# Performance work log

Hardware: AMD Instinct MI355X
Metric: run time of the kernel (lower is better)

## Reference

```python
import jax, jax.numpy as jnp
import numpy as np

DIM = 512
NUM_HEADS = 16
WIN = (7, 7)
SIZE = WIN[0] * WIN[1]  # 49
B = 2048   # total windows
NW = 4     # windows per image (mask groups)


def _relative_position_index():
    coords_h = np.arange(WIN[0])
    coords_w = np.arange(WIN[1])
    coords = np.stack(np.meshgrid(coords_h, coords_w, indexing='ij'))  # [2,Wh,Ww]
    flat = coords.reshape(2, -1)                                       # [2,S]
    rel = flat[:, :, None] - flat[:, None, :]                          # [2,S,S]
    rel = rel.transpose(1, 2, 0)                                       # [S,S,2]
    rel[:, :, 0] += WIN[0] - 1
    rel[:, :, 1] += WIN[1] - 1
    rel[:, :, 0] *= 2 * WIN[1] - 1
    return rel.sum(-1).astype(np.int32)                                # [S,S]


def setup_inputs() -> dict:
    key = jax.random.key(0)
    ks = jax.random.split(key, 8)
    num_bias = (2 * WIN[0] - 1) * (2 * WIN[1] - 1)  # 169
    sd = 1.0 / np.sqrt(DIM)
    return {
        'x': jax.random.normal(ks[0], (B, SIZE, DIM), dtype=jnp.float32),
        'mask': jax.random.normal(ks[1], (NW, SIZE, SIZE), dtype=jnp.float32),
        'w_qkv': jax.random.normal(ks[2], (DIM, 3 * DIM), dtype=jnp.float32) * sd,
        'b_qkv': jnp.zeros((3 * DIM,), dtype=jnp.float32),
        'w_proj': jax.random.normal(ks[3], (DIM, DIM), dtype=jnp.float32) * sd,
        'b_proj': jnp.zeros((DIM,), dtype=jnp.float32),
        'bias_table': jax.random.normal(ks[4], (num_bias, NUM_HEADS), dtype=jnp.float32) * 0.02,
        'rel_idx': jnp.asarray(_relative_position_index()),
    }


def reference(x, mask, w_qkv, b_qkv, w_proj, b_proj, bias_table, rel_idx):
    b, s, c = x.shape
    h = NUM_HEADS
    hd = c // h
    scale = hd ** (-0.5)
    # qkv projection -> [3, B, H, S, hd]
    qkv = (x @ w_qkv + b_qkv).reshape(b, s, 3, h, hd).transpose(2, 0, 3, 1, 4)
    q, k, v = qkv[0] * scale, qkv[1], qkv[2]
    attn = jnp.einsum('bhqd,bhkd->bhqk', q, k)                 # [B,H,S,S]
    # gathered relative position bias -> [H,S,S]
    bias = bias_table[rel_idx.reshape(-1)].reshape(s, s, h).transpose(2, 0, 1)
    attn = attn + bias[None]
    nw = mask.shape[0]
    attn = attn.reshape(b // nw, nw, h, s, s) + mask[None, :, None]
    attn = jax.nn.softmax(attn.reshape(b, h, s, s), axis=-1)
    out = jnp.einsum('bhqk,bhkd->bhqd', attn, v)               # [B,H,S,hd]
    out = out.transpose(0, 2, 1, 3).reshape(b, s, c)
    return out @ w_proj + b_proj
```

## Files before the change

### kernel.cpp

```cpp
#include <hip/hip_runtime.h>
#include <hip/hip_bf16.h>
#include <stdint.h>

typedef float  floatx4 __attribute__((ext_vector_type(4)));
typedef short  short8  __attribute__((ext_vector_type(8)));
typedef unsigned short u16;

#define DIM 512
#define NH 16
#define HD 32
#define WS 49
#define NBW 2048
#define NWIN 4
#define M_TOTAL (NBW*WS)
#define N_QKV (3*DIM)

__device__ __forceinline__ u16 f2bf(float f) {
    uint32_t u = __float_as_uint(f);
    u += 0x7FFFu + ((u >> 16) & 1u);
    return (u16)(u >> 16);
}

__device__ __forceinline__ void load_lds16(const u16* g, u16* l) {
    __builtin_amdgcn_global_load_lds(
        (const __attribute__((address_space(1))) unsigned int*)g,
        (__attribute__((address_space(3))) unsigned int*)l, 16, 0, 0);
}

__global__ void cast_x_kernel(const float* __restrict__ in, u16* __restrict__ out, int n4) {
    int i = blockIdx.x * blockDim.x + threadIdx.x;
    if (i >= n4) return;
    const float4 v = ((const float4*)in)[i];
    ushort4 o;
    o.x = f2bf(v.x); o.y = f2bf(v.y); o.z = f2bf(v.z); o.w = f2bf(v.w);
    ((ushort4*)out)[i] = o;
}

__global__ void transpose_cast_kernel(const float* __restrict__ in, u16* __restrict__ out,
                                      int N, int total) {
    int idx = blockIdx.x * blockDim.x + threadIdx.x;
    if (idx >= total) return;
    int k = idx & (DIM - 1);
    int n = idx >> 9;
    out[idx] = f2bf(in[k * N + n]);
}

__global__ void build_comb_kernel(const float* __restrict__ bias_table, const int* __restrict__ rel_idx,
                                  const float* __restrict__ mask, float* __restrict__ comb) {
    int idx = blockIdx.x * blockDim.x + threadIdx.x;
    if (idx >= NWIN * NH * 64 * 64) return;
    int j = idx & 63, i = (idx >> 6) & 63, h = (idx >> 12) & 15, g = idx >> 16;
    float v = -1e30f;
    if (i < WS && j < WS)
        v = bias_table[rel_idx[i * WS + j] * NH + h] + mask[(g * WS + i) * WS + j];
    comb[idx] = v;
}

template<bool OUT_BF16>
__global__ __launch_bounds__(256, 2) void gemm_bt_kernel(
    const u16* __restrict__ A, const u16* __restrict__ Bt,
    const float* __restrict__ bias, void* __restrict__ out, int N, int K)
{
    __shared__ __align__(16) u16 sA[128 * 32];
    __shared__ __align__(16) u16 sB[128 * 32];
    const int tid  = threadIdx.x;
    const int lane = tid & 63;
    const int wave = tid >> 6;
    const long m0 = (long)blockIdx.y * 128;
    const long n0 = (long)blockIdx.x * 128;
    const int rr = lane & 15;
    const int qk = (lane >> 4) * 8;
    const int wm = (wave >> 1) * 64;
    const int wn = (wave & 1) * 64;

    floatx4 acc[4][4];
    const floatx4 z4 = {0.f, 0.f, 0.f, 0.f};
#pragma unroll
    for (int mi = 0; mi < 4; ++mi)
#pragma unroll
        for (int ni = 0; ni < 4; ++ni) acc[mi][ni] = z4;

    const int row0 = tid >> 2;
    const int kc0  = (tid & 3) * 8;
    const u16* gA0 = A  + (m0 + row0) * K + kc0;
    const u16* gA1 = A  + (m0 + row0 + 64) * K + kc0;
    const u16* gB0 = Bt + (n0 + row0) * K + kc0;
    const u16* gB1 = Bt + (n0 + row0 + 64) * K + kc0;
    u16* lA0 = sA + tid * 8;
    u16* lA1 = sA + (tid + 256) * 8;
    u16* lB0 = sB + tid * 8;
    u16* lB1 = sB + (tid + 256) * 8;

    for (int k0 = 0; k0 < K; k0 += 32) {
        load_lds16(gA0 + k0, lA0);
        load_lds16(gA1 + k0, lA1);
        load_lds16(gB0 + k0, lB0);
        load_lds16(gB1 + k0, lB1);
        __syncthreads();
        short8 af[4], bfr[4];
#pragma unroll
        for (int mi = 0; mi < 4; ++mi)
            af[mi] = *(const short8*)(sA + (wm + mi * 16 + rr) * 32 + qk);
#pragma unroll
        for (int ni = 0; ni < 4; ++ni)
            bfr[ni] = *(const short8*)(sB + (wn + ni * 16 + rr) * 32 + qk);
#pragma unroll
        for (int mi = 0; mi < 4; ++mi)
#pragma unroll
            for (int ni = 0; ni < 4; ++ni)
                acc[mi][ni] = __builtin_amdgcn_mfma_f32_16x16x32_bf16(af[mi], bfr[ni], acc[mi][ni], 0, 0, 0);
        __syncthreads();
    }

#pragma unroll
    for (int mi = 0; mi < 4; ++mi) {
#pragma unroll
        for (int r = 0; r < 4; ++r) {
            const long m = m0 + wm + mi * 16 + (lane >> 4) * 4 + r;
#pragma unroll
            for (int ni = 0; ni < 4; ++ni) {
                const long n = n0 + wn + ni * 16 + rr;
                float v = acc[mi][ni][r] + bias[n];
                if (OUT_BF16) ((u16*)out)[m * N + n] = f2bf(v);
                else          ((float*)out)[m * N + n] = v;
            }
        }
    }
}

__global__ __launch_bounds__(64, 4) void attn_kernel(
    const u16* __restrict__ qkv, const float* __restrict__ comb,
    u16* __restrict__ attn_out)
{
    const int bh = blockIdx.x;
    const int b = bh >> 4, h = bh & 15;
    const int l = threadIdx.x;
    const int rr = l & 15;
    const int q4 = l >> 4;
    const int qk = q4 * 8;

    __shared__ __align__(16) u16 p_s[64 * 64];

    const u16* qg = qkv + (long)b * WS * N_QKV + h * HD;
    const u16* kg = qg + DIM;
    const u16* vg = qg + 2 * DIM;

    short8 af[4], bfr[4];
    const short8 z8 = {0, 0, 0, 0, 0, 0, 0, 0};
#pragma unroll
    for (int mi = 0; mi < 4; ++mi) {
        const int row = mi * 16 + rr;
        af[mi] = (row < WS) ? *(const short8*)(qg + (long)row * N_QKV + qk) : z8;
    }
#pragma unroll
    for (int ni = 0; ni < 4; ++ni) {
        const int row = ni * 16 + rr;
        bfr[ni] = (row < WS) ? *(const short8*)(kg + (long)row * N_QKV + qk) : z8;
    }

    floatx4 sc[4][4];
    const floatx4 z4 = {0.f, 0.f, 0.f, 0.f};
#pragma unroll
    for (int mi = 0; mi < 4; ++mi)
#pragma unroll
        for (int ni = 0; ni < 4; ++ni)
            sc[mi][ni] = __builtin_amdgcn_mfma_f32_16x16x32_bf16(af[mi], bfr[ni], z4, 0, 0, 0);

    short8 vf[2][2];
#pragma unroll
    for (int kk = 0; kk < 2; ++kk)
#pragma unroll
        for (int ni = 0; ni < 2; ++ni) {
            short8 t = z8;
            const int d = ni * 16 + rr;
#pragma unroll
            for (int j = 0; j < 8; ++j) {
                const int s = kk * 32 + qk + j;
                if (s < WS) t[j] = (short)vg[(long)s * N_QKV + d];
            }
            vf[kk][ni] = t;
        }

    const float* cb = comb + (long)((b & (NWIN - 1)) * NH + h) * 4096;
    const float scale = 0.17677669529663689f;
    float inv_s[4][4];
#pragma unroll
    for (int mi = 0; mi < 4; ++mi) {
#pragma unroll
        for (int r = 0; r < 4; ++r) {
            const int i = mi * 16 + q4 * 4 + r;
            float s0 = sc[mi][0][r] * scale + cb[i * 64 +  0 + rr];
            float s1 = sc[mi][1][r] * scale + cb[i * 64 + 16 + rr];
            float s2 = sc[mi][2][r] * scale + cb[i * 64 + 32 + rr];
            float s3 = sc[mi][3][r] * scale + cb[i * 64 + 48 + rr];
            float mx = fmaxf(fmaxf(s0, s1), fmaxf(s2, s3));
#pragma unroll
            for (int off = 1; off < 16; off <<= 1) mx = fmaxf(mx, __shfl_xor(mx, off, 64));
            float e0 = __expf(s0 - mx), e1 = __expf(s1 - mx);
            float e2 = __expf(s2 - mx), e3 = __expf(s3 - mx);
            float sm = e0 + e1 + e2 + e3;
#pragma unroll
            for (int off = 1; off < 16; off <<= 1) sm += __shfl_xor(sm, off, 64);
            inv_s[mi][r] = 1.0f / sm;
#pragma unroll
            for (int c = 0; c < 4; ++c) {
                const int col = c * 16 + rr;
                const int blk = (col >> 3) ^ (i & 7);
                const float ev = (c == 0) ? e0 : (c == 1) ? e1 : (c == 2) ? e2 : e3;
                p_s[i * 64 + blk * 8 + (col & 7)] = f2bf(ev);
            }
        }
    }
    __syncthreads();

    floatx4 oacc[4][2];
#pragma unroll
    for (int mi = 0; mi < 4; ++mi) { oacc[mi][0] = z4; oacc[mi][1] = z4; }
#pragma unroll
    for (int kk = 0; kk < 2; ++kk) {
        short8 pf[4];
#pragma unroll
        for (int mi = 0; mi < 4; ++mi) {
            const int i2 = mi * 16 + rr;
            pf[mi] = *(const short8*)(p_s + i2 * 64 + (((4 * kk + q4) ^ (i2 & 7)) * 8));
        }
#pragma unroll
        for (int mi = 0; mi < 4; ++mi)
#pragma unroll
            for (int ni = 0; ni < 2; ++ni)
                oacc[mi][ni] = __builtin_amdgcn_mfma_f32_16x16x32_bf16(pf[mi], vf[kk][ni], oacc[mi][ni], 0, 0, 0);
    }

#pragma unroll
    for (int mi = 0; mi < 4; ++mi) {
#pragma unroll
        for (int r = 0; r < 4; ++r) {
            const int i = mi * 16 + q4 * 4 + r;
            if (i < WS) {
                const float inv = inv_s[mi][r];
                u16* op = attn_out + ((long)(b * WS + i)) * DIM + h * HD;
                op[rr]      = f2bf(oacc[mi][0][r] * inv);
                op[16 + rr] = f2bf(oacc[mi][1][r] * inv);
            }
        }
    }
}

extern "C" void kernel_launch(void* const* d_in, const int* in_sizes, int n_in,
                              void* d_out, int out_size, void* d_ws, size_t ws_size,
                              hipStream_t stream)
{
    const float* x          = (const float*)d_in[0];
    const float* mask       = (const float*)d_in[1];
    const float* w_qkv      = (const float*)d_in[2];
    const float* b_qkv      = (const float*)d_in[3];
    const float* w_proj     = (const float*)d_in[4];
    const float* b_proj     = (const float*)d_in[5];
    const float* bias_table = (const float*)d_in[6];
    const int*   rel_idx    = (const int*)d_in[7];
    float* out = (float*)d_out;

    char* ws = (char*)d_ws;
    u16* x_bf   = (u16*)ws;  ws += (size_t)M_TOTAL * DIM * 2;
    u16* wqkvT  = (u16*)ws;  ws += (size_t)N_QKV * DIM * 2;
    u16* wprojT = (u16*)ws;  ws += (size_t)DIM * DIM * 2;
    float* comb = (float*)ws; ws += (size_t)NWIN * NH * 64 * 64 * 4;
    u16* qkv    = (u16*)ws;  ws += (size_t)M_TOTAL * N_QKV * 2;
    u16* attn_o = x_bf;

    const int n4 = M_TOTAL * DIM / 4;
    cast_x_kernel<<<(n4 + 255) / 256, 256, 0, stream>>>(x, x_bf, n4);
    transpose_cast_kernel<<<(N_QKV * DIM + 255) / 256, 256, 0, stream>>>(w_qkv, wqkvT, N_QKV, N_QKV * DIM);
    transpose_cast_kernel<<<(DIM * DIM + 255) / 256, 256, 0, stream>>>(w_proj, wprojT, DIM, DIM * DIM);
    build_comb_kernel<<<(NWIN * NH * 64 * 64 + 255) / 256, 256, 0, stream>>>(bias_table, rel_idx, mask, comb);

    gemm_bt_kernel<true><<<dim3(N_QKV / 128, M_TOTAL / 128), 256, 0, stream>>>(
        x_bf, wqkvT, b_qkv, qkv, N_QKV, DIM);

    attn_kernel<<<NBW * NH, 64, 0, stream>>>(qkv, comb, attn_o);

    gemm_bt_kernel<false><<<dim3(DIM / 128, M_TOTAL / 128), 256, 0, stream>>>(
        attn_o, wprojT, b_proj, out, DIM, DIM);
}
```

Before: 905.7 us.

## Split attention per half-window per wave, drop max-subtraction, compute row sums via MFMA

The attention kernel now gives each wave half the query rows of one (window, head) pair and packs four waves per block. This halves per-wave register and LDS use and replaces the block barrier with an LDS wait. Softmax no longer subtracts the row max, and the row sum comes from an extra MFMA against a ones vector instead of shuffle reductions. The comb table is reordered so each lane reads a float4, and the output stores are packed into 32-bit words. Skipping max-subtraction risks exp overflow with larger logits, and K and V fragments are now loaded twice per window.

After: 856.5 us. 1.06x faster.

```diff
diff --git a/kernel.cpp b/kernel.cpp
--- a/kernel.cpp
+++ b/kernel.cpp
@@ -49,7 +49,8 @@
                                   const float* __restrict__ mask, float* __restrict__ comb) {
     int idx = blockIdx.x * blockDim.x + threadIdx.x;
     if (idx >= NWIN * NH * 64 * 64) return;
-    int j = idx & 63, i = (idx >> 6) & 63, h = (idx >> 12) & 15, g = idx >> 16;
+    int c = idx & 3, jj = (idx >> 2) & 15, i = (idx >> 6) & 63, h = (idx >> 12) & 15, g = idx >> 16;
+    int j = c * 16 + jj;
     float v = -1e30f;
     if (i < WS && j < WS)
         v = bias_table[rel_idx[i * WS + j] * NH + h] + mask[(g * WS + i) * WS + j];
@@ -128,28 +129,35 @@
     }
 }
 
-__global__ __launch_bounds__(64, 4) void attn_kernel(
+__global__ __launch_bounds__(256, 4) void attn_kernel(
     const u16* __restrict__ qkv, const float* __restrict__ comb,
     u16* __restrict__ attn_out)
 {
-    const int bh = blockIdx.x;
-    const int b = bh >> 4, h = bh & 15;
-    const int l = threadIdx.x;
+    const int w   = threadIdx.x >> 6;
+    const int l   = threadIdx.x & 63;
+    const int job = blockIdx.x * 4 + w;
+    const int b    = job >> 5;
+    const int h    = (job >> 1) & 15;
+    const int half = job & 1;
+    const int row0 = half * 32;
     const int rr = l & 15;
     const int q4 = l >> 4;
     const int qk = q4 * 8;
 
-    __shared__ __align__(16) u16 p_s[64 * 64];
+    __shared__ __align__(16) u16 p_s[4][32 * 64];
+    u16* ps = p_s[w];
 
     const u16* qg = qkv + (long)b * WS * N_QKV + h * HD;
     const u16* kg = qg + DIM;
     const u16* vg = qg + 2 * DIM;
 
-    short8 af[4], bfr[4];
     const short8 z8 = {0, 0, 0, 0, 0, 0, 0, 0};
-#pragma unroll
-    for (int mi = 0; mi < 4; ++mi) {
-        const int row = mi * 16 + rr;
+    const floatx4 z4 = {0.f, 0.f, 0.f, 0.f};
+
+    short8 af[2], bfr[4];
+#pragma unroll
+    for (int mi = 0; mi < 2; ++mi) {
+        const int row = row0 + mi * 16 + rr;
         af[mi] = (row < WS) ? *(const short8*)(qg + (long)row * N_QKV + qk) : z8;
     }
 #pragma unroll
@@ -158,21 +166,13 @@
         bfr[ni] = (row < WS) ? *(const short8*)(kg + (long)row * N_QKV + qk) : z8;
     }
 
-    floatx4 sc[4][4];
-    const floatx4 z4 = {0.f, 0.f, 0.f, 0.f};
-#pragma unroll
-    for (int mi = 0; mi < 4; ++mi)
-#pragma unroll
-        for (int ni = 0; ni < 4; ++ni)
-            sc[mi][ni] = __builtin_amdgcn_mfma_f32_16x16x32_bf16(af[mi], bfr[ni], z4, 0, 0, 0);
-
     short8 vf[2][2];
 #pragma unroll
     for (int kk = 0; kk < 2; ++kk)
 #pragma unroll
         for (int ni = 0; ni < 2; ++ni) {
             short8 t = z8;
-            const int d = ni * 16 + rr;
+            const int d = 2 * rr + ni;
 #pragma unroll
             for (int j = 0; j < 8; ++j) {
                 const int s = kk * 32 + qk + j;
@@ -180,67 +180,70 @@
             }
             vf[kk][ni] = t;
         }
-
-    const float* cb = comb + (long)((b & (NWIN - 1)) * NH + h) * 4096;
+    short8 vones;
+#pragma unroll
+    for (int j = 0; j < 8; ++j) vones[j] = (short)0x3F80;
+
+    floatx4 sc[2][4];
+#pragma unroll
+    for (int mi = 0; mi < 2; ++mi)
+#pragma unroll
+        for (int ni = 0; ni < 4; ++ni)
+            sc[mi][ni] = __builtin_amdgcn_mfma_f32_16x16x32_bf16(af[mi], bfr[ni], z4, 0, 0, 0);
+
+    const float4* cb4 = (const float4*)comb + ((long)((b & (NWIN - 1)) * NH + h)) * 1024;
     const float scale = 0.17677669529663689f;
-    float inv_s[4][4];
-#pragma unroll
-    for (int mi = 0; mi < 4; ++mi) {
+#pragma unroll
+    for (int mi = 0; mi < 2; ++mi) {
 #pragma unroll
         for (int r = 0; r < 4; ++r) {
-            const int i = mi * 16 + q4 * 4 + r;
-            float s0 = sc[mi][0][r] * scale + cb[i * 64 +  0 + rr];
-            float s1 = sc[mi][1][r] * scale + cb[i * 64 + 16 + rr];
-            float s2 = sc[mi][2][r] * scale + cb[i * 64 + 32 + rr];
-            float s3 = sc[mi][3][r] * scale + cb[i * 64 + 48 + rr];
-            float mx = fmaxf(fmaxf(s0, s1), fmaxf(s2, s3));
-#pragma unroll
-            for (int off = 1; off < 16; off <<= 1) mx = fmaxf(mx, __shfl_xor(mx, off, 64));
-            float e0 = __expf(s0 - mx), e1 = __expf(s1 - mx);
-            float e2 = __expf(s2 - mx), e3 = __expf(s3 - mx);
-            float sm = e0 + e1 + e2 + e3;
-#pragma unroll
-            for (int off = 1; off < 16; off <<= 1) sm += __shfl_xor(sm, off, 64);
-            inv_s[mi][r] = 1.0f / sm;
+            const int il = mi * 16 + q4 * 4 + r;
+            const float4 cb = cb4[(row0 + il) * 16 + rr];
+            float e0 = __expf(sc[mi][0][r] * scale + cb.x);
+            float e1 = __expf(sc[mi][1][r] * scale + cb.y);
+            float e2 = __expf(sc[mi][2][r] * scale + cb.z);
+            float e3 = __expf(sc[mi][3][r] * scale + cb.w);
 #pragma unroll
             for (int c = 0; c < 4; ++c) {
                 const int col = c * 16 + rr;
-                const int blk = (col >> 3) ^ (i & 7);
+                const int blk = (col >> 3) ^ (il & 7);
                 const float ev = (c == 0) ? e0 : (c == 1) ? e1 : (c == 2) ? e2 : e3;
-                p_s[i * 64 + blk * 8 + (col & 7)] = f2bf(ev);
-            }
-        }
-    }
-    __syncthreads();
-
-    floatx4 oacc[4][2];
-#pragma unroll
-    for (int mi = 0; mi < 4; ++mi) { oacc[mi][0] = z4; oacc[mi][1] = z4; }
+                ps[il * 64 + blk * 8 + (col & 7)] = f2bf(ev);
+            }
+        }
+    }
+    asm volatile("s_waitcnt lgkmcnt(0)" ::: "memory");
+
+    floatx4 oacc[2][3];
+#pragma unroll
+    for (int mi = 0; mi < 2; ++mi) { oacc[mi][0] = z4; oacc[mi][1] = z4; oacc[mi][2] = z4; }
 #pragma unroll
     for (int kk = 0; kk < 2; ++kk) {
-        short8 pf[4];
-#pragma unroll
-        for (int mi = 0; mi < 4; ++mi) {
+        short8 pf[2];
+#pragma unroll
+        for (int mi = 0; mi < 2; ++mi) {
             const int i2 = mi * 16 + rr;
-            pf[mi] = *(const short8*)(p_s + i2 * 64 + (((4 * kk + q4) ^ (i2 & 7)) * 8));
-        }
-#pragma unroll
-        for (int mi = 0; mi < 4; ++mi)
-#pragma unroll
-            for (int ni = 0; ni < 2; ++ni)
-                oacc[mi][ni] = __builtin_amdgcn_mfma_f32_16x16x32_bf16(pf[mi], vf[kk][ni], oacc[mi][ni], 0, 0, 0);
-    }
-
-#pragma unroll
-    for (int mi = 0; mi < 4; ++mi) {
+            pf[mi] = *(const short8*)(ps + i2 * 64 + (((4 * kk + q4) ^ (i2 & 7)) * 8));
+        }
+#pragma unroll
+        for (int mi = 0; mi < 2; ++mi) {
+            oacc[mi][0] = __builtin_amdgcn_mfma_f32_16x16x32_bf16(pf[mi], vf[kk][0], oacc[mi][0], 0, 0, 0);
+            oacc[mi][1] = __builtin_amdgcn_mfma_f32_16x16x32_bf16(pf[mi], vf[kk][1], oacc[mi][1], 0, 0, 0);
+            oacc[mi][2] = __builtin_amdgcn_mfma_f32_16x16x32_bf16(pf[mi], vones,     oacc[mi][2], 0, 0, 0);
+        }
+    }
+
+#pragma unroll
+    for (int mi = 0; mi < 2; ++mi) {
 #pragma unroll
         for (int r = 0; r < 4; ++r) {
-            const int i = mi * 16 + q4 * 4 + r;
-            if (i < WS) {
-                const float inv = inv_s[mi][r];
-                u16* op = attn_out + ((long)(b * WS + i)) * DIM + h * HD;
-                op[rr]      = f2bf(oacc[mi][0][r] * inv);
-                op[16 + rr] = f2bf(oacc[mi][1][r] * inv);
+            const int ig = row0 + mi * 16 + q4 * 4 + r;
+            if (ig < WS) {
+                const float inv = 1.0f / oacc[mi][2][r];
+                const uint32_t lo = f2bf(oacc[mi][0][r] * inv);
+                const uint32_t hi = f2bf(oacc[mi][1][r] * inv);
+                uint32_t* op = (uint32_t*)(attn_out + ((long)(b * WS + ig)) * DIM + h * HD);
+                op[rr] = lo | (hi << 16);
             }
         }
     }
@@ -277,7 +280,7 @@
     gemm_bt_kernel<true><<<dim3(N_QKV / 128, M_TOTAL / 128), 256, 0, stream>>>(
         x_bf, wqkvT, b_qkv, qkv, N_QKV, DIM);
 
-    attn_kernel<<<NBW * NH, 64, 0, stream>>>(qkv, comb, attn_o);
+    attn_kernel<<<NBW * NH * 2 / 4, 256, 0, stream>>>(qkv, comb, attn_o);
 
     gemm_bt_kernel<false><<<dim3(DIM / 128, M_TOTAL / 128), 256, 0, stream>>>(
         attn_o, wprojT, b_proj, out, DIM, DIM);
```
